# Kernel tuning notes

Hardware: AMD Instinct MI355X
Metric: run time of the kernel (lower is better)

## Reference

```python
import jax, jax.numpy as jnp
import numpy as np

N_NODES = 10000
N_EDGES = 320000
HIDDEN = 128
MIX = 8


def setup_inputs() -> dict:
    key = jax.random.key(0)
    k1, k2, k3, k4 = jax.random.split(key, 4)
    X = jax.random.normal(k1, (N_NODES, HIDDEN), dtype=jnp.float32)
    # nn.Linear default init scale ~ 1/sqrt(fan_in)
    W_A = jax.random.normal(k2, (HIDDEN, HIDDEN), dtype=jnp.float32) / np.sqrt(HIDDEN)
    W_B = jax.random.normal(k3, (MIX, HIDDEN), dtype=jnp.float32) / np.sqrt(HIDDEN)
    edge_index = jax.random.randint(k4, (2, N_EDGES), 0, N_NODES, dtype=jnp.int64)
    return {"X": X, "W_A": W_A, "W_B": W_B, "edge_index": edge_index, "num_nodes": N_NODES}


def reference(X, W_A, W_B, edge_index, num_nodes):
    src, dst = edge_index[0], edge_index[1]
    X_src = X[src]                                            # (E, h) gather
    # hyper-network weights per edge: W_B(gelu(W_A(x)))  -> (E, mix)
    W_tar_edge = jax.nn.gelu(X_src @ W_A.T, approximate=False) @ W_B.T
    # edge-wise outer product (E, h, mix)
    cross = X_src[:, :, None] * W_tar_edge[:, None, :]
    # scatter-add into node bins (N, h, mix)
    agg = jnp.zeros((num_nodes, X.shape[1], W_tar_edge.shape[1]), dtype=X.dtype)
    agg = agg.at[dst].add(cross)
    agg = jax.nn.gelu(agg, approximate=False)
    # gather back per edge and contract over mix dim -> (E, h)
    out_edge = jnp.einsum('ehm,em->eh', agg[dst], W_tar_edge)
    return (out_edge, src, dst)
```

## Files before the change

### kernel.cpp

```cpp
#include <hip/hip_runtime.h>
#include <hip/hip_bf16.h>

#define HIDDEN 128
#define MIX 8

#define NBW 32
#define LDX 33
#define KT  16
#define LDW 17
#define LDG 132

__device__ __forceinline__ float gelu_exact(float x) {
    return 0.5f * x * (1.0f + erff(x * 0.7071067811865476f));
}

__global__ __launch_bounds__(256) void k_wnode(const float* __restrict__ X,
                                               const float* __restrict__ W_A,
                                               const float* __restrict__ W_B,
                                               float* __restrict__ Wnode,
                                               int N) {
    __shared__ float xs[NBW * LDX];
    __shared__ float wa[HIDDEN * LDW];
    __shared__ float gsm[NBW * LDG];
    __shared__ float wb[MIX * LDG];

    int t = threadIdx.x;
    int n0 = blockIdx.x * NBW;

    {
        int r = t >> 3;
        int c0 = (t & 7) * 16;
        int rn = n0 + r; if (rn >= N) rn = N - 1;
        const float* xp = X + (size_t)rn * HIDDEN + c0;
        float4 a = ((const float4*)xp)[0];
        float4 b = ((const float4*)xp)[1];
        float4 c = ((const float4*)xp)[2];
        float4 d = ((const float4*)xp)[3];
        float tmp[16] = {a.x,a.y,a.z,a.w, b.x,b.y,b.z,b.w,
                         c.x,c.y,c.z,c.w, d.x,d.y,d.z,d.w};
#pragma unroll
        for (int q = 0; q < 16; ++q) xs[r * LDX + c0 + q] = tmp[q];
    }

    int ngrp = t & 7;
    int jgrp = t >> 3;
    float acc[4][4];
#pragma unroll
    for (int i = 0; i < 4; ++i)
#pragma unroll
        for (int j = 0; j < 4; ++j) acc[i][j] = 0.f;

    for (int kt = 0; kt < HIDDEN; kt += KT) {
        __syncthreads();
        {
            int j = t >> 1;
            int c0 = (t & 1) * 8;
            const float* wp = W_A + (size_t)j * HIDDEN + kt + c0;
            float4 a = ((const float4*)wp)[0];
            float4 b = ((const float4*)wp)[1];
            float tmp[8] = {a.x,a.y,a.z,a.w, b.x,b.y,b.z,b.w};
#pragma unroll
            for (int q = 0; q < 8; ++q) wa[j * LDW + c0 + q] = tmp[q];
        }
        __syncthreads();
#pragma unroll
        for (int k = 0; k < KT; ++k) {
            float xv[4], wv[4];
#pragma unroll
            for (int i = 0; i < 4; ++i) xv[i] = xs[(ngrp * 4 + i) * LDX + kt + k];
#pragma unroll
            for (int j = 0; j < 4; ++j) wv[j] = wa[(jgrp * 4 + j) * LDW + k];
#pragma unroll
            for (int i = 0; i < 4; ++i)
#pragma unroll
                for (int j = 0; j < 4; ++j) acc[i][j] += xv[i] * wv[j];
        }
    }

#pragma unroll
    for (int i = 0; i < 4; ++i)
#pragma unroll
        for (int j = 0; j < 4; ++j)
            gsm[(ngrp * 4 + i) * LDG + (jgrp * 4 + j)] = gelu_exact(acc[i][j]);

    if (t < 64) {
        int r = t >> 3;
        int c0 = (t & 7) * 16;
        const float* wp = W_B + (size_t)r * HIDDEN + c0;
        float4 a = ((const float4*)wp)[0];
        float4 b = ((const float4*)wp)[1];
        float4 c = ((const float4*)wp)[2];
        float4 d = ((const float4*)wp)[3];
        float tmp[16] = {a.x,a.y,a.z,a.w, b.x,b.y,b.z,b.w,
                         c.x,c.y,c.z,c.w, d.x,d.y,d.z,d.w};
#pragma unroll
        for (int q = 0; q < 16; ++q) wb[r * LDG + c0 + q] = tmp[q];
    }
    __syncthreads();

    {
        int n = t >> 3;
        int m = t & 7;
        float a = 0.f;
#pragma unroll 8
        for (int k = 0; k < HIDDEN; ++k)
            a += gsm[n * LDG + k] * wb[m * LDG + k];
        if (n0 + n < N) Wnode[(size_t)n0 * MIX + t] = a;
    }
}

__global__ __launch_bounds__(256) void k_hist(const int* __restrict__ src,
                                              const int* __restrict__ dst,
                                              int* __restrict__ counts,
                                              float* __restrict__ out_src,
                                              float* __restrict__ out_dst,
                                              int E) {
    int e = blockIdx.x * 256 + threadIdx.x;
    if (e < E) {
        int d = dst[e];
        atomicAdd(&counts[d], 1);
        out_src[e] = (float)src[e];
        out_dst[e] = (float)d;
    }
}

__global__ __launch_bounds__(1024) void k_scan(const int* __restrict__ counts,
                                               int* __restrict__ offsets,
                                               int N) {
    __shared__ int ls[1024];
    int t = threadIdx.x;
    int chunk = (N + 1023) / 1024;
    int begin = t * chunk;
    int end = begin + chunk; if (end > N) end = N;
    int s = 0;
    for (int i = begin; i < end; ++i) s += counts[i];
    ls[t] = s;
    __syncthreads();
    for (int off = 1; off < 1024; off <<= 1) {
        int v = (t >= off) ? ls[t - off] : 0;
        __syncthreads();
        ls[t] += v;
        __syncthreads();
    }
    int run = (t == 0) ? 0 : ls[t - 1];
    for (int i = begin; i < end; ++i) { offsets[i] = run; run += counts[i]; }
    if (t == 1023) offsets[N] = run;
}

__global__ __launch_bounds__(256) void k_fill(const int* __restrict__ dst,
                                              int* __restrict__ cursor,
                                              const int* __restrict__ offsets,
                                              int* __restrict__ csr,
                                              int E) {
    int e = blockIdx.x * 256 + threadIdx.x;
    if (e < E) {
        int d = dst[e];
        int p = atomicAdd(&cursor[d], 1);
        csr[offsets[d] + p] = e;
    }
}

__global__ __launch_bounds__(256) void k_node(const float* __restrict__ X,
                                              const float* __restrict__ Wnode,
                                              const int* __restrict__ src,
                                              const int* __restrict__ csr,
                                              const int* __restrict__ offsets,
                                              float* __restrict__ out_edge,
                                              int N) {
    int lane = threadIdx.x & 63;
    int n = blockIdx.x * 4 + (threadIdx.x >> 6);
    if (n >= N) return;
    int beg = offsets[n];
    int cnt = offsets[n + 1] - beg;
    if (cnt == 0) return;

    float ag0[MIX], ag1[MIX];
#pragma unroll
    for (int m = 0; m < MIX; ++m) { ag0[m] = 0.f; ag1[m] = 0.f; }

    for (int c0 = 0; c0 < cnt; c0 += 64) {
        int nb = min(64, cnt - c0);
        int idx = c0 + ((lane < nb) ? lane : 0);
        int e_l = csr[beg + idx];
        int s_l = src[e_l];
#pragma unroll 2
        for (int i = 0; i < nb; ++i) {
            int s = __builtin_amdgcn_readlane(s_l, i);
            const float* wp = Wnode + (size_t)s * MIX;
            float2 x = ((const float2*)(X + (size_t)s * HIDDEN))[lane];
#pragma unroll
            for (int m = 0; m < MIX; ++m) {
                float w = wp[m];
                ag0[m] += x.x * w;
                ag1[m] += x.y * w;
            }
        }
    }

#pragma unroll
    for (int m = 0; m < MIX; ++m) {
        ag0[m] = gelu_exact(ag0[m]);
        ag1[m] = gelu_exact(ag1[m]);
    }

    for (int c0 = 0; c0 < cnt; c0 += 64) {
        int nb = min(64, cnt - c0);
        int idx = c0 + ((lane < nb) ? lane : 0);
        int e_l = csr[beg + idx];
        int s_l = src[e_l];
#pragma unroll 2
        for (int i = 0; i < nb; ++i) {
            int s = __builtin_amdgcn_readlane(s_l, i);
            int e = __builtin_amdgcn_readlane(e_l, i);
            const float* wp = Wnode + (size_t)s * MIX;
            float2 o;
            o.x = ag0[0]*wp[0] + ag0[1]*wp[1] + ag0[2]*wp[2] + ag0[3]*wp[3]
                + ag0[4]*wp[4] + ag0[5]*wp[5] + ag0[6]*wp[6] + ag0[7]*wp[7];
            o.y = ag1[0]*wp[0] + ag1[1]*wp[1] + ag1[2]*wp[2] + ag1[3]*wp[3]
                + ag1[4]*wp[4] + ag1[5]*wp[5] + ag1[6]*wp[6] + ag1[7]*wp[7];
            ((float2*)(out_edge + (size_t)e * HIDDEN))[lane] = o;
        }
    }
}

extern "C" void kernel_launch(void* const* d_in, const int* in_sizes, int n_in,
                              void* d_out, int out_size, void* d_ws, size_t ws_size,
                              hipStream_t stream) {
    const float* X   = (const float*)d_in[0];
    const float* W_A = (const float*)d_in[1];
    const float* W_B = (const float*)d_in[2];
    const int*   ei  = (const int*)d_in[3];

    const int N = in_sizes[0] / HIDDEN;
    const int E = in_sizes[3] / 2;
    const int* src = ei;
    const int* dst = ei + E;

    float* out      = (float*)d_out;
    float* out_edge = out;
    float* out_src  = out + (size_t)E * HIDDEN;
    float* out_dst  = out_src + E;

    int* counts  = (int*)d_ws;
    int* cursor  = counts + N;
    int* offsets = cursor + N;
    int* csr     = offsets + (N + 1);
    float* Wnode = (float*)(csr + E);

    hipMemsetAsync(counts, 0, sizeof(int) * (size_t)(2 * N), stream);

    k_wnode<<<(N + NBW - 1) / NBW, 256, 0, stream>>>(X, W_A, W_B, Wnode, N);

    int eb = (E + 255) / 256;
    k_hist<<<eb, 256, 0, stream>>>(src, dst, counts, out_src, out_dst, E);
    k_scan<<<1, 1024, 0, stream>>>(counts, offsets, N);
    k_fill<<<eb, 256, 0, stream>>>(dst, cursor, offsets, csr, E);
    k_node<<<(N + 3) / 4, 256, 0, stream>>>(X, Wnode, src, csr, offsets, out_edge, N);
}
```

Baseline: 280.6 us.

## Merge histogram into Wnode kernel, replace serial scan with atomic block allocation

```diff
diff --git a/kernel.cpp b/kernel.cpp
--- a/kernel.cpp
+++ b/kernel.cpp
@@ -1,5 +1,4 @@
 #include <hip/hip_runtime.h>
-#include <hip/hip_bf16.h>
 
 #define HIDDEN 128
 #define MIX 8
@@ -10,21 +9,40 @@
 #define LDW 17
 #define LDG 132
 
+typedef float v2f __attribute__((ext_vector_type(2)));
+
 __device__ __forceinline__ float gelu_exact(float x) {
     return 0.5f * x * (1.0f + erff(x * 0.7071067811865476f));
 }
 
-__global__ __launch_bounds__(256) void k_wnode(const float* __restrict__ X,
-                                               const float* __restrict__ W_A,
-                                               const float* __restrict__ W_B,
-                                               float* __restrict__ Wnode,
-                                               int N) {
+__global__ __launch_bounds__(256) void k_prep(const float* __restrict__ X,
+                                              const float* __restrict__ W_A,
+                                              const float* __restrict__ W_B,
+                                              float* __restrict__ Wnode,
+                                              const int* __restrict__ src,
+                                              const int* __restrict__ dst,
+                                              int* __restrict__ counts,
+                                              float* __restrict__ out_src,
+                                              float* __restrict__ out_dst,
+                                              int N, int E, int WB) {
+    int t = threadIdx.x;
+
+    if ((int)blockIdx.x >= WB) {
+        int e = ((int)blockIdx.x - WB) * 256 + t;
+        if (e < E) {
+            int d = dst[e];
+            atomicAdd(&counts[d], 1);
+            __builtin_nontemporal_store((float)src[e], &out_src[e]);
+            __builtin_nontemporal_store((float)d, &out_dst[e]);
+        }
+        return;
+    }
+
     __shared__ float xs[NBW * LDX];
     __shared__ float wa[HIDDEN * LDW];
     __shared__ float gsm[NBW * LDG];
     __shared__ float wb[MIX * LDG];
 
-    int t = threadIdx.x;
     int n0 = blockIdx.x * NBW;
 
     {
@@ -109,42 +127,30 @@
     }
 }
 
-__global__ __launch_bounds__(256) void k_hist(const int* __restrict__ src,
-                                              const int* __restrict__ dst,
-                                              int* __restrict__ counts,
-                                              float* __restrict__ out_src,
-                                              float* __restrict__ out_dst,
-                                              int E) {
-    int e = blockIdx.x * 256 + threadIdx.x;
-    if (e < E) {
-        int d = dst[e];
-        atomicAdd(&counts[d], 1);
-        out_src[e] = (float)src[e];
-        out_dst[e] = (float)d;
-    }
-}
-
-__global__ __launch_bounds__(1024) void k_scan(const int* __restrict__ counts,
+__global__ __launch_bounds__(256) void k_alloc(const int* __restrict__ counts,
                                                int* __restrict__ offsets,
-                                               int N) {
-    __shared__ int ls[1024];
+                                               int* __restrict__ acur, int N) {
     int t = threadIdx.x;
-    int chunk = (N + 1023) / 1024;
-    int begin = t * chunk;
-    int end = begin + chunk; if (end > N) end = N;
-    int s = 0;
-    for (int i = begin; i < end; ++i) s += counts[i];
-    ls[t] = s;
+    int lane = t & 63, wid = t >> 6;
+    int n = blockIdx.x * 256 + t;
+    int c = (n < N) ? counts[n] : 0;
+    int v = c;
+#pragma unroll
+    for (int off = 1; off < 64; off <<= 1) {
+        int u = __shfl_up(v, off, 64);
+        if (lane >= off) v += u;
+    }
+    __shared__ int wsum[4], wbase[4], bbase;
+    if (lane == 63) wsum[wid] = v;
     __syncthreads();
-    for (int off = 1; off < 1024; off <<= 1) {
-        int v = (t >= off) ? ls[t - off] : 0;
-        __syncthreads();
-        ls[t] += v;
-        __syncthreads();
-    }
-    int run = (t == 0) ? 0 : ls[t - 1];
-    for (int i = begin; i < end; ++i) { offsets[i] = run; run += counts[i]; }
-    if (t == 1023) offsets[N] = run;
+    if (t == 0) {
+        int s = 0;
+#pragma unroll
+        for (int w = 0; w < 4; ++w) { wbase[w] = s; s += wsum[w]; }
+        bbase = atomicAdd(acur, s);
+    }
+    __syncthreads();
+    if (n < N) offsets[n] = bbase + wbase[wid] + (v - c);
 }
 
 __global__ __launch_bounds__(256) void k_fill(const int* __restrict__ dst,
@@ -165,13 +171,14 @@
                                               const int* __restrict__ src,
                                               const int* __restrict__ csr,
                                               const int* __restrict__ offsets,
+                                              const int* __restrict__ counts,
                                               float* __restrict__ out_edge,
                                               int N) {
     int lane = threadIdx.x & 63;
     int n = blockIdx.x * 4 + (threadIdx.x >> 6);
     if (n >= N) return;
     int beg = offsets[n];
-    int cnt = offsets[n + 1] - beg;
+    int cnt = counts[n];
     if (cnt == 0) return;
 
     float ag0[MIX], ag1[MIX];
@@ -183,7 +190,7 @@
         int idx = c0 + ((lane < nb) ? lane : 0);
         int e_l = csr[beg + idx];
         int s_l = src[e_l];
-#pragma unroll 2
+#pragma unroll 4
         for (int i = 0; i < nb; ++i) {
             int s = __builtin_amdgcn_readlane(s_l, i);
             const float* wp = Wnode + (size_t)s * MIX;
@@ -208,17 +215,17 @@
         int idx = c0 + ((lane < nb) ? lane : 0);
         int e_l = csr[beg + idx];
         int s_l = src[e_l];
-#pragma unroll 2
+#pragma unroll 4
         for (int i = 0; i < nb; ++i) {
             int s = __builtin_amdgcn_readlane(s_l, i);
             int e = __builtin_amdgcn_readlane(e_l, i);
             const float* wp = Wnode + (size_t)s * MIX;
-            float2 o;
+            v2f o;
             o.x = ag0[0]*wp[0] + ag0[1]*wp[1] + ag0[2]*wp[2] + ag0[3]*wp[3]
                 + ag0[4]*wp[4] + ag0[5]*wp[5] + ag0[6]*wp[6] + ag0[7]*wp[7];
             o.y = ag1[0]*wp[0] + ag1[1]*wp[1] + ag1[2]*wp[2] + ag1[3]*wp[3]
                 + ag1[4]*wp[4] + ag1[5]*wp[5] + ag1[6]*wp[6] + ag1[7]*wp[7];
-            ((float2*)(out_edge + (size_t)e * HIDDEN))[lane] = o;
+            __builtin_nontemporal_store(o, (v2f*)(out_edge + (size_t)e * HIDDEN) + lane);
         }
     }
 }
@@ -243,17 +250,20 @@
 
     int* counts  = (int*)d_ws;
     int* cursor  = counts + N;
-    int* offsets = cursor + N;
-    int* csr     = offsets + (N + 1);
+    int* acur    = cursor + N;
+    int* offsets = acur + 4;
+    int* csr     = offsets + N;
     float* Wnode = (float*)(csr + E);
 
-    hipMemsetAsync(counts, 0, sizeof(int) * (size_t)(2 * N), stream);
-
-    k_wnode<<<(N + NBW - 1) / NBW, 256, 0, stream>>>(X, W_A, W_B, Wnode, N);
-
-    int eb = (E + 255) / 256;
-    k_hist<<<eb, 256, 0, stream>>>(src, dst, counts, out_src, out_dst, E);
-    k_scan<<<1, 1024, 0, stream>>>(counts, offsets, N);
-    k_fill<<<eb, 256, 0, stream>>>(dst, cursor, offsets, csr, E);
-    k_node<<<(N + 3) / 4, 256, 0, stream>>>(X, Wnode, src, csr, offsets, out_edge, N);
-}
+    hipMemsetAsync(counts, 0, sizeof(int) * (size_t)(2 * N + 4), stream);
+
+    int WB = (N + NBW - 1) / NBW;
+    int EB = (E + 255) / 256;
+
+    k_prep<<<WB + EB, 256, 0, stream>>>(X, W_A, W_B, Wnode, src, dst,
+                                        counts, out_src, out_dst, N, E, WB);
+    k_alloc<<<(N + 255) / 256, 256, 0, stream>>>(counts, offsets, acur, N);
+    k_fill<<<EB, 256, 0, stream>>>(dst, cursor, offsets, csr, E);
+    k_node<<<(N + 3) / 4, 256, 0, stream>>>(X, Wnode, src, csr, offsets, counts,
+                                            out_edge, N);
+}
```

After: 270.0 us. -3.8%, faster.
